# Kernel tuning notes

Measured on AMD Instinct MI355X. Metric: run time of the kernel, lower is better.

## Reference

```python
import jax, jax.numpy as jnp
from jax import lax
import numpy as np

EPS = 1e-5

def setup_inputs() -> dict:
    key = jax.random.key(0)
    k1, k2, k3, k4 = jax.random.split(key, 4)
    B, in_c, out_c, k, z_dim, H, W = 16, 128, 256, 3, 256, 64, 64
    fan_in = in_c * k * k
    x = jax.random.normal(k1, (B, in_c, H, W), dtype=jnp.float32)
    z = jax.random.normal(k2, (B, z_dim), dtype=jnp.float32)
    base_weight = jax.random.normal(k3, (out_c, in_c, k, k), dtype=jnp.float32) * np.sqrt(2.0 / fan_in)
    head_w = jax.random.normal(k4, (out_c * in_c * k * k, z_dim), dtype=jnp.float32) * np.sqrt(1.0 / z_dim)
    return {"x": x, "z": z, "base_weight": base_weight, "head_w": head_w}

def reference(x, z, base_weight, head_w):
    # x: [B, in_c, H, W]; z: [B, z_dim]; base_weight: [out_c, in_c, k, k]; head_w: [out_c*in_c*k*k, z_dim]
    B = x.shape[0]
    out_c, in_c, k, _ = base_weight.shape
    fan_in = in_c * k * k
    hyper_weight = 1.0

    # delta_w = Linear(z) -> [B, out_c, in_c, k, k]
    delta_w = jnp.einsum('bz,oz->bo', z, head_w).reshape(B, out_c, in_c, k, k)
    # standardize over (in_c, k, k) per (sample, out-channel)
    mu = jnp.mean(delta_w, axis=(2, 3, 4), keepdims=True)
    var = jnp.var(delta_w, axis=(2, 3, 4), keepdims=True)
    delta_w = (delta_w - mu) * lax.rsqrt(var + EPS)
    delta_w = delta_w * jnp.sqrt(2.0 / fan_in)

    w = (base_weight[None] + hyper_weight * delta_w) / jnp.sqrt(2.0)  # [B, out_c, in_c, k, k]

    pad = k // 2
    def conv_one(xb, wb):
        # xb: [in_c, H, W], wb: [out_c, in_c, k, k]
        return lax.conv_general_dilated(
            xb[None], wb, window_strides=(1, 1), padding=[(pad, pad), (pad, pad)],
            dimension_numbers=('NCHW', 'OIHW', 'NCHW'))[0]

    out = jax.vmap(conv_one)(x, w)  # [B, out_c, H_out, W_out]
    return out
```

## Files before the change

kernel.cpp:

```cpp
#include <hip/hip_runtime.h>

#define B_  16
#define IC  128
#define OC  256
#define ZD  256
#define HH  64
#define WW  64
#define FAN 1152
#define NO  294912
#define HP  66

typedef float    fvec4 __attribute__((ext_vector_type(4)));
typedef _Float16 f16x8 __attribute__((ext_vector_type(8)));
typedef _Float16 f16x4 __attribute__((ext_vector_type(4)));

__global__ __launch_bounds__(256) void delta_gemm_kernel(
    const float* __restrict__ z, const float* __restrict__ head_w,
    float* __restrict__ delta) {
  __shared__ _Float16 As[256 * 40];
  __shared__ _Float16 zsh[16 * 264];
  int t = threadIdx.x;
  int row0 = blockIdx.x * 256;
  int lane = t & 63, wave = t >> 6;
  int quad = lane >> 4, l16 = lane & 15;

  for (int u = t; u < 1024; u += 256) {
    int b = u >> 6, kq = u & 63;
    fvec4 v = *(const fvec4*)&z[b * 256 + kq * 4];
    f16x4 h = {(_Float16)v.x, (_Float16)v.y, (_Float16)v.z, (_Float16)v.w};
    *(f16x4*)&zsh[b * 264 + kq * 4] = h;
  }

  fvec4 acc[4];
#pragma unroll
  for (int i = 0; i < 4; ++i) acc[i] = (fvec4){0.f, 0.f, 0.f, 0.f};

  int srow_lo = t >> 3;
  int skq = t & 7;

  for (int zc = 0; zc < 8; ++zc) {
    __syncthreads();
#pragma unroll
    for (int i = 0; i < 8; ++i) {
      int row = i * 32 + srow_lo;
      fvec4 v = *(const fvec4*)&head_w[(size_t)(row0 + row) * 256 + zc * 32 + skq * 4];
      f16x4 h = {(_Float16)v.x, (_Float16)v.y, (_Float16)v.z, (_Float16)v.w};
      *(f16x4*)&As[row * 40 + skq * 4] = h;
    }
    __syncthreads();
    f16x8 bfz = *(const f16x8*)&zsh[l16 * 264 + zc * 32 + quad * 8];
#pragma unroll
    for (int mt = 0; mt < 4; ++mt) {
      f16x8 af = *(const f16x8*)&As[(wave * 64 + mt * 16 + l16) * 40 + quad * 8];
      acc[mt] = __builtin_amdgcn_mfma_f32_16x16x32_f16(af, bfz, acc[mt], 0, 0, 0);
    }
  }
#pragma unroll
  for (int mt = 0; mt < 4; ++mt) {
    int gr = row0 + wave * 64 + mt * 16 + quad * 4;
#pragma unroll
    for (int r = 0; r < 4; ++r)
      delta[(size_t)l16 * NO + gr + r] = acc[mt][r];
  }
}

__global__ __launch_bounds__(256) void standardize_kernel(
    const float* __restrict__ delta, const float* __restrict__ base_w,
    _Float16* __restrict__ w_h) {
  int b  = blockIdx.x >> 8;
  int oc = blockIdx.x & 255;
  int tid = threadIdx.x;
  const float* d = delta + (size_t)b * NO + oc * FAN;

  float s = 0.f, s2 = 0.f;
  for (int j = tid; j < FAN; j += 256) { float v = d[j]; s += v; s2 += v * v; }
#pragma unroll
  for (int off = 32; off > 0; off >>= 1) {
    s  += __shfl_down(s, off);
    s2 += __shfl_down(s2, off);
  }
  __shared__ float rs[4], rq[4];
  if ((tid & 63) == 0) { rs[tid >> 6] = s; rq[tid >> 6] = s2; }
  __syncthreads();
  float S  = rs[0] + rs[1] + rs[2] + rs[3];
  float S2 = rq[0] + rq[1] + rq[2] + rq[3];
  const float inv_fan = 1.0f / (float)FAN;
  float mu  = S * inv_fan;
  float var = S2 * inv_fan - mu * mu;
  const float inv_sqrt2 = 0.70710678118654752f;
  float sc = rsqrtf(var + 1e-5f) * sqrtf(2.0f / (float)FAN) * inv_sqrt2;

  const float* bw = base_w + oc * FAN;
  _Float16* wp = w_h + ((size_t)b * OC + oc) * FAN;
  for (int i = tid; i < FAN; i += 256) {
    int ic = i & 127, kk = i >> 7;
    int j = ic * 9 + kk;
    float val = bw[j] * inv_sqrt2 + (d[j] - mu) * sc;
    wp[i] = (_Float16)val;
  }
}

__global__ __launch_bounds__(256) void xpose_kernel(
    const float* __restrict__ x, _Float16* __restrict__ x_h) {
  int yp = blockIdx.x;
  int b  = blockIdx.y;
  int t  = threadIdx.x;
  _Float16* orow = x_h + ((size_t)(b * HP + yp)) * HP * IC;

  if (yp == 0 || yp == HP - 1) {
    fvec4 zz = (fvec4){0.f, 0.f, 0.f, 0.f};
    for (int u = t; u < HP * IC / 8; u += 256)
      ((fvec4*)orow)[u] = zz;
    return;
  }
  int y = yp - 1;
  __shared__ float tile[128 * 65];
#pragma unroll
  for (int i = 0; i < 8; ++i) {
    int F = i * 256 + t;
    int ic = F >> 4, xq = F & 15;
    fvec4 v = *(const fvec4*)&x[(((size_t)b * IC + ic) * HH + y) * WW + xq * 4];
    float* tp = &tile[ic * 65 + xq * 4];
    tp[0] = v.x; tp[1] = v.y; tp[2] = v.z; tp[3] = v.w;
  }
  __syncthreads();
#pragma unroll
  for (int j = 0; j < 4; ++j) {
    int u = j * 256 + t;
    int px = u >> 4, icg = u & 15;
    _Float16 h[8];
#pragma unroll
    for (int c = 0; c < 8; ++c) h[c] = (_Float16)tile[(icg * 8 + c) * 65 + px];
    *(f16x8*)&orow[(px + 1) * IC + icg * 8] = *(f16x8*)h;
  }
  if (t < 32) {
    int side = t >> 4, icg = t & 15;
    fvec4 zz = (fvec4){0.f, 0.f, 0.f, 0.f};
    *(fvec4*)&orow[(side ? (HP - 1) * IC : 0) + icg * 8] = zz;
  }
}

__global__ __launch_bounds__(256) void conv_mfma_kernel(
    const _Float16* __restrict__ x_h, const _Float16* __restrict__ w_h,
    float* __restrict__ out) {
  __shared__ _Float16 As[128 * 72];
  __shared__ _Float16 Bs[128 * 72];
  int t = threadIdx.x;
  int b = blockIdx.z;
  int oc0 = blockIdx.y * 128;
  int y0 = blockIdx.x * 2;
  int lane = t & 63, wave = t >> 6;
  int wm = wave >> 1, wn = wave & 1;
  int quad = lane >> 4, l16 = lane & 15;

  fvec4 acc[4][4];
#pragma unroll
  for (int i = 0; i < 4; ++i)
#pragma unroll
    for (int j = 0; j < 4; ++j) acc[i][j] = (fvec4){0.f, 0.f, 0.f, 0.f};

  int srow = t >> 1;
  int half = t & 1;
  const _Float16* wbase = w_h + ((size_t)(b * OC + oc0 + srow)) * FAN + half * 32;
  int ry = srow >> 6, xx = srow & 63;

  for (int kk = 0; kk < 9; ++kk) {
    int ky = kk / 3, kx = kk % 3;
    int yp = y0 + ry + ky;
    int xp = xx + kx;
    const _Float16* xbase =
        x_h + (((size_t)(b * HP + yp)) * HP + xp) * IC + half * 32;
#pragma unroll
    for (int icc = 0; icc < 2; ++icc) {
      const fvec4* asrc = (const fvec4*)(wbase + kk * 128 + icc * 64);
      const fvec4* bsrc = (const fvec4*)(xbase + icc * 64);
      fvec4 a0 = asrc[0], a1 = asrc[1], a2 = asrc[2], a3 = asrc[3];
      fvec4 b0 = bsrc[0], b1 = bsrc[1], b2 = bsrc[2], b3 = bsrc[3];
      __syncthreads();
      fvec4* adst = (fvec4*)(As + srow * 72 + half * 32);
      adst[0] = a0; adst[1] = a1; adst[2] = a2; adst[3] = a3;
      fvec4* bdst = (fvec4*)(Bs + srow * 72 + half * 32);
      bdst[0] = b0; bdst[1] = b1; bdst[2] = b2; bdst[3] = b3;
      __syncthreads();
#pragma unroll
      for (int ks = 0; ks < 2; ++ks) {
        f16x8 af[4], bf[4];
#pragma unroll
        for (int i = 0; i < 4; ++i)
          af[i] = *(const f16x8*)&As[(wm * 64 + i * 16 + l16) * 72 + ks * 32 + quad * 8];
#pragma unroll
        for (int j = 0; j < 4; ++j)
          bf[j] = *(const f16x8*)&Bs[(wn * 64 + j * 16 + l16) * 72 + ks * 32 + quad * 8];
#pragma unroll
        for (int i = 0; i < 4; ++i)
#pragma unroll
          for (int j = 0; j < 4; ++j)
            acc[i][j] = __builtin_amdgcn_mfma_f32_16x16x32_f16(af[i], bf[j], acc[i][j], 0, 0, 0);
      }
    }
  }

#pragma unroll
  for (int i = 0; i < 4; ++i)
#pragma unroll
    for (int j = 0; j < 4; ++j) {
      int m  = oc0 + wm * 64 + i * 16 + quad * 4;
      int nn = wn * 64 + j * 16 + l16;
      int oy = y0 + (nn >> 6), ox = nn & 63;
      float* op = out + (((size_t)(b * OC + m) * HH + oy) * WW + ox);
#pragma unroll
      for (int r = 0; r < 4; ++r)
        op[(size_t)r * HH * WW] = acc[i][j][r];
    }
}

extern "C" void kernel_launch(void* const* d_in, const int* in_sizes, int n_in,
                              void* d_out, int out_size, void* d_ws, size_t ws_size,
                              hipStream_t stream) {
  const float* x      = (const float*)d_in[0];
  const float* z      = (const float*)d_in[1];
  const float* base_w = (const float*)d_in[2];
  const float* head_w = (const float*)d_in[3];
  float* out = (float*)d_out;

  _Float16* w_h   = (_Float16*)d_ws;
  float*    delta = (float*)((char*)d_ws + (size_t)B_ * OC * FAN * sizeof(_Float16));
  _Float16* x_h   = (_Float16*)delta;

  delta_gemm_kernel<<<NO / 256, 256, 0, stream>>>(z, head_w, delta);
  standardize_kernel<<<B_ * OC, 256, 0, stream>>>(delta, base_w, w_h);
  xpose_kernel<<<dim3(HP, B_), 256, 0, stream>>>(x, x_h);
  conv_mfma_kernel<<<dim3(32, 2, B_), 256, 0, stream>>>(x_h, w_h, out);
}
```

Baseline: 514.9 us.

## Load conv MFMA operands directly from global memory and widen delta GEMM K-chunk

The conv kernel drops its LDS staging and barriers: each wave loads its A (weights) and B (input pixels) MFMA fragments straight from global memory, with the 3x3 loop fully unrolled. This removes the shared-memory round trip and __syncthreads. In exchange, each block re-reads data across waves and relies on L1/L2 for reuse, which raises global load traffic and latency exposure. Separately, the delta GEMM now stages 64-wide z chunks per iteration instead of 32, halving its barrier count at the cost of more LDS.

```diff
diff --git a/kernel.cpp b/kernel.cpp
--- a/kernel.cpp
+++ b/kernel.cpp
@@ -17,7 +17,7 @@
 __global__ __launch_bounds__(256) void delta_gemm_kernel(
     const float* __restrict__ z, const float* __restrict__ head_w,
     float* __restrict__ delta) {
-  __shared__ _Float16 As[256 * 40];
+  __shared__ _Float16 As[256 * 72];
   __shared__ _Float16 zsh[16 * 264];
   int t = threadIdx.x;
   int row0 = blockIdx.x * 256;
@@ -35,24 +35,27 @@
 #pragma unroll
   for (int i = 0; i < 4; ++i) acc[i] = (fvec4){0.f, 0.f, 0.f, 0.f};
 
-  int srow_lo = t >> 3;
-  int skq = t & 7;
-
-  for (int zc = 0; zc < 8; ++zc) {
+  int srow_lo = t >> 4;
+  int sseg = t & 15;
+
+  for (int zc2 = 0; zc2 < 4; ++zc2) {
     __syncthreads();
 #pragma unroll
-    for (int i = 0; i < 8; ++i) {
-      int row = i * 32 + srow_lo;
-      fvec4 v = *(const fvec4*)&head_w[(size_t)(row0 + row) * 256 + zc * 32 + skq * 4];
+    for (int i = 0; i < 16; ++i) {
+      int row = i * 16 + srow_lo;
+      fvec4 v = *(const fvec4*)&head_w[(size_t)(row0 + row) * 256 + zc2 * 64 + sseg * 4];
       f16x4 h = {(_Float16)v.x, (_Float16)v.y, (_Float16)v.z, (_Float16)v.w};
-      *(f16x4*)&As[row * 40 + skq * 4] = h;
+      *(f16x4*)&As[row * 72 + sseg * 4] = h;
     }
     __syncthreads();
-    f16x8 bfz = *(const f16x8*)&zsh[l16 * 264 + zc * 32 + quad * 8];
-#pragma unroll
-    for (int mt = 0; mt < 4; ++mt) {
-      f16x8 af = *(const f16x8*)&As[(wave * 64 + mt * 16 + l16) * 40 + quad * 8];
-      acc[mt] = __builtin_amdgcn_mfma_f32_16x16x32_f16(af, bfz, acc[mt], 0, 0, 0);
+#pragma unroll
+    for (int kc = 0; kc < 2; ++kc) {
+      f16x8 bfz = *(const f16x8*)&zsh[l16 * 264 + zc2 * 64 + kc * 32 + quad * 8];
+#pragma unroll
+      for (int mt = 0; mt < 4; ++mt) {
+        f16x8 af = *(const f16x8*)&As[(wave * 64 + mt * 16 + l16) * 72 + kc * 32 + quad * 8];
+        acc[mt] = __builtin_amdgcn_mfma_f32_16x16x32_f16(af, bfz, acc[mt], 0, 0, 0);
+      }
     }
   }
 #pragma unroll
@@ -143,8 +146,6 @@
 __global__ __launch_bounds__(256) void conv_mfma_kernel(
     const _Float16* __restrict__ x_h, const _Float16* __restrict__ w_h,
     float* __restrict__ out) {
-  __shared__ _Float16 As[128 * 72];
-  __shared__ _Float16 Bs[128 * 72];
   int t = threadIdx.x;
   int b = blockIdx.z;
   int oc0 = blockIdx.y * 128;
@@ -159,43 +160,33 @@
 #pragma unroll
     for (int j = 0; j < 4; ++j) acc[i][j] = (fvec4){0.f, 0.f, 0.f, 0.f};
 
-  int srow = t >> 1;
-  int half = t & 1;
-  const _Float16* wbase = w_h + ((size_t)(b * OC + oc0 + srow)) * FAN + half * 32;
-  int ry = srow >> 6, xx = srow & 63;
-
-  for (int kk = 0; kk < 9; ++kk) {
-    int ky = kk / 3, kx = kk % 3;
-    int yp = y0 + ry + ky;
-    int xp = xx + kx;
-    const _Float16* xbase =
-        x_h + (((size_t)(b * HP + yp)) * HP + xp) * IC + half * 32;
-#pragma unroll
-    for (int icc = 0; icc < 2; ++icc) {
-      const fvec4* asrc = (const fvec4*)(wbase + kk * 128 + icc * 64);
-      const fvec4* bsrc = (const fvec4*)(xbase + icc * 64);
-      fvec4 a0 = asrc[0], a1 = asrc[1], a2 = asrc[2], a3 = asrc[3];
-      fvec4 b0 = bsrc[0], b1 = bsrc[1], b2 = bsrc[2], b3 = bsrc[3];
-      __syncthreads();
-      fvec4* adst = (fvec4*)(As + srow * 72 + half * 32);
-      adst[0] = a0; adst[1] = a1; adst[2] = a2; adst[3] = a3;
-      fvec4* bdst = (fvec4*)(Bs + srow * 72 + half * 32);
-      bdst[0] = b0; bdst[1] = b1; bdst[2] = b2; bdst[3] = b3;
-      __syncthreads();
-#pragma unroll
-      for (int ks = 0; ks < 2; ++ks) {
-        f16x8 af[4], bf[4];
-#pragma unroll
-        for (int i = 0; i < 4; ++i)
-          af[i] = *(const f16x8*)&As[(wm * 64 + i * 16 + l16) * 72 + ks * 32 + quad * 8];
-#pragma unroll
-        for (int j = 0; j < 4; ++j)
-          bf[j] = *(const f16x8*)&Bs[(wn * 64 + j * 16 + l16) * 72 + ks * 32 + quad * 8];
-#pragma unroll
-        for (int i = 0; i < 4; ++i)
+  const _Float16* ap = w_h + ((size_t)(b * OC + oc0 + wm * 64 + l16)) * FAN + quad * 8;
+  const _Float16* bp = x_h + (((size_t)(b * HP + y0 + wn)) * HP + l16) * IC + quad * 8;
+
+#pragma unroll
+  for (int ky = 0; ky < 3; ++ky) {
+#pragma unroll
+    for (int kx = 0; kx < 3; ++kx) {
+      int kk = ky * 3 + kx;
+      const _Float16* apk = ap + kk * 128;
+      const _Float16* bpk = bp + (ky * HP + kx) * IC;
+#pragma unroll
+      for (int icc = 0; icc < 2; ++icc) {
+#pragma unroll
+        for (int ks = 0; ks < 2; ++ks) {
+          f16x8 af[4], bf[4];
+#pragma unroll
+          for (int i = 0; i < 4; ++i)
+            af[i] = *(const f16x8*)(apk + i * (16 * FAN) + icc * 64 + ks * 32);
 #pragma unroll
           for (int j = 0; j < 4; ++j)
-            acc[i][j] = __builtin_amdgcn_mfma_f32_16x16x32_f16(af[i], bf[j], acc[i][j], 0, 0, 0);
+            bf[j] = *(const f16x8*)(bpk + j * (16 * IC) + icc * 64 + ks * 32);
+#pragma unroll
+          for (int i = 0; i < 4; ++i)
+#pragma unroll
+            for (int j = 0; j < 4; ++j)
+              acc[i][j] = __builtin_amdgcn_mfma_f32_16x16x32_f16(af[i], bf[j], acc[i][j], 0, 0, 0);
+        }
       }
     }
   }
```

New measurement: 589.5 us. 14.5% more time.
